# Performance work log

Measured on AMD Instinct MI355X. Metric: run time of the kernel, lower is better.

Reference implementation:

```python
import jax, jax.numpy as jnp
import numpy as np

B, S, D = 2, 2048, 1024  # batch, seq, model_dim
E, K, H = 8, 2, 4096     # experts, top_k, expert hidden
CAP_FACTOR = 1.0


def setup_inputs() -> dict:
    key = jax.random.key(0)
    ks = jax.random.split(key, 6)
    scale_in = 1.0 / np.sqrt(D)
    scale_h = 1.0 / np.sqrt(H)
    return {
        "x": jax.random.normal(ks[0], (B, S, D), jnp.float32),
        "wg": jax.random.normal(ks[1], (D, E), jnp.float32) * scale_in,
        "w1": jax.random.normal(ks[2], (E, D, H), jnp.float32) * scale_in,
        "b1": jnp.zeros((E, H), jnp.float32),
        "w2": jax.random.normal(ks[3], (E, H, D), jnp.float32) * scale_h,
        "b2": jnp.zeros((E, D), jnp.float32),
    }


def _moe_forward(x, wg, w1, b1, w2, b2):
    Bb, Ss, Dd = x.shape
    T = Bb * Ss
    cap = int(K * CAP_FACTOR * ((T + E - 1) // E))  # Tutel capacity rule
    xt = x.reshape(T, Dd)

    # ---- gating ----
    logits = xt @ wg                      # [T, E]
    scores = jax.nn.softmax(logits, axis=-1)
    gates_k, idx_k = jax.lax.top_k(scores, K)  # [T, K]
    # normalize_gate=True: renormalize top-k gates
    gates_k = gates_k / jnp.sum(gates_k, axis=-1, keepdims=True)

    # ---- GShard-style location assignment (slot-major cumsum) ----
    masks = jax.nn.one_hot(idx_k, E, dtype=jnp.int32)           # [T, K, E]
    m = jnp.transpose(masks, (1, 0, 2)).reshape(K * T, E)       # slot-major
    locs_full = jnp.cumsum(m, axis=0) - 1                       # [K*T, E]
    loc = jnp.sum(locs_full * m, axis=-1)                       # [K*T]
    loc = loc.reshape(K, T).T                                   # [T, K]
    valid = (loc < cap).astype(xt.dtype)                        # capacity drop
    loc_c = jnp.clip(loc, 0, cap - 1)

    # ---- dispatch: scatter tokens into [E, cap, D] ----
    contrib = (xt[:, None, :] * valid[:, :, None]).reshape(T * K, Dd)
    disp = jnp.zeros((E, cap, Dd), xt.dtype)
    disp = disp.at[idx_k.reshape(-1), loc_c.reshape(-1)].add(contrib)

    # ---- grouped expert FFN ----
    h = jax.nn.relu(jnp.einsum("ecd,edh->ech", disp, w1) + b1[:, None, :])
    out = jnp.einsum("ech,ehd->ecd", h, w2) + b2[:, None, :]

    # ---- combine (postscore): gather + gate-weighted sum ----
    gathered = out[idx_k, loc_c]                                # [T, K, D]
    y = jnp.einsum("tk,tkd->td", gates_k * valid, gathered)
    return y.reshape(Bb, Ss, Dd)


def reference(x, wg, w1, b1, w2, b2):
    return _moe_forward(x, wg, w1, b1, w2, b2)
```

## Files before the change

### kernel.cpp

```cpp
#include <hip/hip_runtime.h>
#include <stdint.h>

#define NTOK 4096
#define DIM  1024
#define NEXP 8
#define HID  4096
#define CAP  1024

typedef __bf16 bf16x8 __attribute__((ext_vector_type(8)));
typedef float  f32x4  __attribute__((ext_vector_type(4)));

__device__ __forceinline__ unsigned short f2bf(float f) {
  unsigned int u = __float_as_uint(f);
  return (unsigned short)((u + 0x7fffu + ((u >> 16) & 1u)) >> 16);
}

__device__ __forceinline__ void load_lds16(const void* g, void* l) {
  __builtin_amdgcn_global_load_lds(
      (__attribute__((address_space(1))) void*)g,
      (__attribute__((address_space(3))) void*)l,
      16, 0, 0);
}

__global__ void gating_kernel(const float* __restrict__ x, const float* __restrict__ wg,
                              int* __restrict__ tok_e, float* __restrict__ tok_g) {
  const int t = blockIdx.x;
  const int l = threadIdx.x;
  float acc[NEXP];
#pragma unroll
  for (int e = 0; e < NEXP; ++e) acc[e] = 0.f;

  const float4* x4  = (const float4*)(x + (size_t)t * DIM);
  const float4* wg4 = (const float4*)wg;
#pragma unroll
  for (int i = 0; i < 4; ++i) {
    int dq = i * 64 + l;
    float4 xv = x4[dq];
    float xs[4] = {xv.x, xv.y, xv.z, xv.w};
#pragma unroll
    for (int c = 0; c < 4; ++c) {
      int d = dq * 4 + c;
      float4 wa = wg4[d * 2], wb = wg4[d * 2 + 1];
      acc[0] += xs[c] * wa.x; acc[1] += xs[c] * wa.y;
      acc[2] += xs[c] * wa.z; acc[3] += xs[c] * wa.w;
      acc[4] += xs[c] * wb.x; acc[5] += xs[c] * wb.y;
      acc[6] += xs[c] * wb.z; acc[7] += xs[c] * wb.w;
    }
  }
#pragma unroll
  for (int off = 32; off; off >>= 1)
#pragma unroll
    for (int e = 0; e < NEXP; ++e) acc[e] += __shfl_xor(acc[e], off);

  if (l == 0) {
    float m = acc[0];
#pragma unroll
    for (int e = 1; e < NEXP; ++e) m = fmaxf(m, acc[e]);
    float p[NEXP];
#pragma unroll
    for (int e = 0; e < NEXP; ++e) p[e] = __expf(acc[e] - m);
    int e0 = 0; float b0 = p[0];
#pragma unroll
    for (int e = 1; e < NEXP; ++e) if (p[e] > b0) { b0 = p[e]; e0 = e; }
    int e1 = -1; float b1v = -1.f;
#pragma unroll
    for (int e = 0; e < NEXP; ++e) if (e != e0 && p[e] > b1v) { b1v = p[e]; e1 = e; }
    float inv = 1.f / (b0 + b1v);
    tok_e[2 * t] = e0; tok_e[2 * t + 1] = e1;
    tok_g[2 * t] = b0 * inv; tok_g[2 * t + 1] = b1v * inv;
  }
}

__global__ void scan_kernel(const int* __restrict__ tok_e, int* __restrict__ tok_loc,
                            int* __restrict__ slot_map) {
  const int l = threadIdx.x;
  const unsigned long long below = (1ull << l) - 1ull;
  int base[NEXP];
#pragma unroll
  for (int e = 0; e < NEXP; ++e) base[e] = 0;

  int nxt = tok_e[((0 * 64 + l) & (NTOK - 1)) * 2 + ((0 * 64 + l) >> 12)];
  for (int it = 0; it < 128; ++it) {
    int e = nxt;
    if (it + 1 < 128) {
      int g2 = (it + 1) * 64 + l;
      nxt = tok_e[(g2 & (NTOK - 1)) * 2 + (g2 >> 12)];
    }
    int loc = 0;
#pragma unroll
    for (int ex = 0; ex < NEXP; ++ex) {
      unsigned long long msk = __ballot(e == ex);
      int off = __popcll(msk & below);
      if (e == ex) loc = base[ex] + off;
      base[ex] += __popcll(msk);
    }
    int g = it * 64 + l;
    int k = g >> 12, t = g & (NTOK - 1);
    bool valid = loc < CAP;
    tok_loc[t * 2 + k] = valid ? loc : -1;
    if (valid) slot_map[e * CAP + loc] = t;
  }
#pragma unroll
  for (int ex = 0; ex < NEXP; ++ex) {
    int c = base[ex] < CAP ? base[ex] : CAP;
    for (int i = c + l; i < CAP; i += 64) slot_map[ex * CAP + i] = -1;
  }
}

__global__ void dispatch_kernel(const float* __restrict__ x, const int* __restrict__ slot_map,
                                unsigned short* __restrict__ disp) {
  const int s = blockIdx.x;
  const int tid = threadIdx.x;
  int t = slot_map[s];
  uint2 o;
  if (t >= 0) {
    float4 v = ((const float4*)(x + (size_t)t * DIM))[tid];
    o.x = (unsigned)f2bf(v.x) | ((unsigned)f2bf(v.y) << 16);
    o.y = (unsigned)f2bf(v.z) | ((unsigned)f2bf(v.w) << 16);
  } else {
    o.x = 0u; o.y = 0u;
  }
  ((uint2*)(disp + (size_t)s * DIM))[tid] = o;
}

__global__ void transpose_cvt(const float* __restrict__ in, unsigned short* __restrict__ out,
                              int R, int C) {
  __shared__ float tile[64][65];
  const int e = blockIdx.z;
  const float* inp = in + (size_t)e * R * C;
  unsigned short* outp = out + (size_t)e * R * C;
  const int c0 = blockIdx.x * 64, r0 = blockIdx.y * 64;
  const int tx = threadIdx.x, ty = threadIdx.y;
#pragma unroll
  for (int i = 0; i < 16; ++i) {
    int r = ty + i * 4;
    tile[r][tx] = inp[(size_t)(r0 + r) * C + c0 + tx];
  }
  __syncthreads();
#pragma unroll
  for (int i = 0; i < 16; ++i) {
    int cl = ty + i * 4;
    outp[(size_t)(c0 + cl) * R + r0 + tx] = f2bf(tile[tx][cl]);
  }
}

template <bool RELU, bool BF16OUT>
__global__ __launch_bounds__(256)
void gemm_kernel(const unsigned short* __restrict__ A, const unsigned short* __restrict__ B,
                 const float* __restrict__ bias, void* __restrict__ Cv, int N, int K) {
  constexpr int M = 1024;
  const int e = blockIdx.z;
  A += (size_t)e * M * K;
  B += (size_t)e * N * K;
  bias += (size_t)e * N;
  const int n0 = blockIdx.x * 128;
  const int m0 = blockIdx.y * 128;
  const int tid = threadIdx.x;
  const int wave = tid >> 6, lane = tid & 63;
  const int wm = wave >> 1, wn = wave & 1;

  __shared__ __align__(16) unsigned short As[128 * 64];
  __shared__ __align__(16) unsigned short Bs[128 * 64];

  const int srow = lane >> 3;
  const int scol = (lane & 7) * 8;
  const unsigned short* gA = A + (size_t)(m0 + wave * 8 + srow) * K + scol;
  const unsigned short* gB = B + (size_t)(n0 + wave * 8 + srow) * K + scol;
  unsigned short* lA = As + (wave * 8) * 64;
  unsigned short* lB = Bs + (wave * 8) * 64;

  f32x4 acc[4][4] = {};

  const int quad = lane >> 4;
  const int arow = (wm * 64 + (lane & 15)) * 64 + quad * 8;
  const int brow = (wn * 64 + (lane & 15)) * 64 + quad * 8;

  for (int k0 = 0; k0 < K; k0 += 64) {
    __syncthreads();
#pragma unroll
    for (int i = 0; i < 4; ++i) {
      load_lds16(gA + (size_t)i * 32 * K, lA + i * 32 * 64);
      load_lds16(gB + (size_t)i * 32 * K, lB + i * 32 * 64);
    }
    gA += 64; gB += 64;
    __syncthreads();
#pragma unroll
    for (int kk = 0; kk < 64; kk += 32) {
      bf16x8 af[4], bfr[4];
#pragma unroll
      for (int i = 0; i < 4; ++i)
        af[i] = *reinterpret_cast<const bf16x8*>(&As[arow + i * 16 * 64 + kk]);
#pragma unroll
      for (int j = 0; j < 4; ++j)
        bfr[j] = *reinterpret_cast<const bf16x8*>(&Bs[brow + j * 16 * 64 + kk]);
#pragma unroll
      for (int i = 0; i < 4; ++i)
#pragma unroll
        for (int j = 0; j < 4; ++j)
          acc[i][j] = __builtin_amdgcn_mfma_f32_16x16x32_bf16(af[i], bfr[j], acc[i][j], 0, 0, 0);
    }
  }

  const int crow = m0 + wm * 64 + quad * 4;
  const int ccol = n0 + wn * 64 + (lane & 15);
  unsigned short* Cb = (unsigned short*)Cv + (size_t)e * M * N;
  float* Cf = (float*)Cv + (size_t)e * M * N;
#pragma unroll
  for (int j = 0; j < 4; ++j) {
    float bj = bias[ccol + j * 16];
#pragma unroll
    for (int i = 0; i < 4; ++i) {
#pragma unroll
      for (int r = 0; r < 4; ++r) {
        float v = acc[i][j][r] + bj;
        if (RELU) v = fmaxf(v, 0.f);
        size_t off = (size_t)(crow + i * 16 + r) * N + (ccol + j * 16);
        if (BF16OUT) Cb[off] = f2bf(v);
        else         Cf[off] = v;
      }
    }
  }
}

__global__ void combine_kernel(const float* __restrict__ outb, const int* __restrict__ tok_e,
                               const int* __restrict__ tok_loc, const float* __restrict__ tok_g,
                               float* __restrict__ y) {
  const int t = blockIdx.x;
  const int tid = threadIdx.x;
  int e0 = tok_e[2 * t], e1 = tok_e[2 * t + 1];
  int l0 = tok_loc[2 * t], l1 = tok_loc[2 * t + 1];
  float g0 = tok_g[2 * t], g1 = tok_g[2 * t + 1];
  float ax = 0.f, ay = 0.f, az = 0.f, aw = 0.f;
  if (l0 >= 0) {
    float4 v = ((const float4*)(outb + ((size_t)e0 * CAP + l0) * DIM))[tid];
    ax += g0 * v.x; ay += g0 * v.y; az += g0 * v.z; aw += g0 * v.w;
  }
  if (l1 >= 0) {
    float4 v = ((const float4*)(outb + ((size_t)e1 * CAP + l1) * DIM))[tid];
    ax += g1 * v.x; ay += g1 * v.y; az += g1 * v.z; aw += g1 * v.w;
  }
  float4 o; o.x = ax; o.y = ay; o.z = az; o.w = aw;
  ((float4*)(y + (size_t)t * DIM))[tid] = o;
}

extern "C" void kernel_launch(void* const* d_in, const int* in_sizes, int n_in,
                              void* d_out, int out_size, void* d_ws, size_t ws_size,
                              hipStream_t stream) {
  const float* x  = (const float*)d_in[0];
  const float* wg = (const float*)d_in[1];
  const float* w1 = (const float*)d_in[2];
  const float* b1 = (const float*)d_in[3];
  const float* w2 = (const float*)d_in[4];
  const float* b2 = (const float*)d_in[5];
  float* y = (float*)d_out;

  char* ws = (char*)d_ws;
  int*   tok_e    = (int*)(ws);
  int*   tok_loc  = (int*)(ws + 32768);
  float* tok_g    = (float*)(ws + 65536);
  int*   slot_map = (int*)(ws + 98304);
  unsigned short* disp = (unsigned short*)(ws + 131072);
  unsigned short* wbuf = (unsigned short*)(ws + 131072 + (16ull << 20));
  unsigned short* h    = (unsigned short*)(ws + 131072 + (80ull << 20));
  float*          outb = (float*)(ws + 131072 + (144ull << 20));

  gating_kernel<<<NTOK, 64, 0, stream>>>(x, wg, tok_e, tok_g);
  scan_kernel<<<1, 64, 0, stream>>>(tok_e, tok_loc, slot_map);
  dispatch_kernel<<<NEXP * CAP, 256, 0, stream>>>(x, slot_map, disp);
  transpose_cvt<<<dim3(HID / 64, DIM / 64, NEXP), dim3(64, 4), 0, stream>>>(w1, wbuf, DIM, HID);
  gemm_kernel<true, true><<<dim3(HID / 128, CAP / 128, NEXP), 256, 0, stream>>>(
      disp, wbuf, b1, h, HID, DIM);
  transpose_cvt<<<dim3(DIM / 64, HID / 64, NEXP), dim3(64, 4), 0, stream>>>(w2, wbuf, HID, DIM);
  gemm_kernel<false, false><<<dim3(DIM / 128, CAP / 128, NEXP), 256, 0, stream>>>(
      h, wbuf, b2, outb, DIM, HID);
  combine_kernel<<<NTOK, 256, 0, stream>>>(outb, tok_e, tok_loc, tok_g, y);
}
```

Before: 586.9 us.

## Double-buffer GEMM LDS, swizzle tile order, vectorize transpose, bf16 expert output

The expert GEMMs now double-buffer their LDS tiles so global-to-LDS loads for the next k-step overlap MFMA work, and they drop one barrier per iteration. Block indices are remapped into patches of four N-tiles to improve L2 reuse. The weight transpose-convert uses float4 loads and packed bf16 stores. The second GEMM writes bf16 instead of fp32, which halves output traffic and the combine's reads at some precision cost.

Measured after the change: 580.3 us. About the same (-1.1%).

```diff
diff --git a/kernel.cpp b/kernel.cpp
--- a/kernel.cpp
+++ b/kernel.cpp
@@ -13,6 +13,10 @@
 __device__ __forceinline__ unsigned short f2bf(float f) {
   unsigned int u = __float_as_uint(f);
   return (unsigned short)((u + 0x7fffu + ((u >> 16) & 1u)) >> 16);
+}
+
+__device__ __forceinline__ float bf2f(unsigned int bits16) {
+  return __uint_as_float(bits16 << 16);
 }
 
 __device__ __forceinline__ void load_lds16(const void* g, void* l) {
@@ -130,44 +134,63 @@
   const float* inp = in + (size_t)e * R * C;
   unsigned short* outp = out + (size_t)e * R * C;
   const int c0 = blockIdx.x * 64, r0 = blockIdx.y * 64;
-  const int tx = threadIdx.x, ty = threadIdx.y;
-#pragma unroll
-  for (int i = 0; i < 16; ++i) {
-    int r = ty + i * 4;
-    tile[r][tx] = inp[(size_t)(r0 + r) * C + c0 + tx];
+  const int t = threadIdx.x;
+#pragma unroll
+  for (int i = 0; i < 4; ++i) {
+    int idx = i * 256 + t;
+    int r = idx >> 4;
+    int c4 = (idx & 15) * 4;
+    float4 v = *(const float4*)(inp + (size_t)(r0 + r) * C + c0 + c4);
+    tile[r][c4 + 0] = v.x; tile[r][c4 + 1] = v.y;
+    tile[r][c4 + 2] = v.z; tile[r][c4 + 3] = v.w;
   }
   __syncthreads();
 #pragma unroll
-  for (int i = 0; i < 16; ++i) {
-    int cl = ty + i * 4;
-    outp[(size_t)(c0 + cl) * R + r0 + tx] = f2bf(tile[tx][cl]);
-  }
-}
-
-template <bool RELU, bool BF16OUT>
+  for (int i = 0; i < 4; ++i) {
+    int idx = i * 256 + t;
+    int c = idx >> 4;
+    int r4 = (idx & 15) * 4;
+    float a = tile[r4 + 0][c], b = tile[r4 + 1][c];
+    float d0 = tile[r4 + 2][c], d1 = tile[r4 + 3][c];
+    uint2 o;
+    o.x = (unsigned)f2bf(a) | ((unsigned)f2bf(b) << 16);
+    o.y = (unsigned)f2bf(d0) | ((unsigned)f2bf(d1) << 16);
+    *(uint2*)(outp + (size_t)(c0 + c) * R + r0 + r4) = o;
+  }
+}
+
+template <bool RELU, int MB, int NB>
 __global__ __launch_bounds__(256)
 void gemm_kernel(const unsigned short* __restrict__ A, const unsigned short* __restrict__ B,
-                 const float* __restrict__ bias, void* __restrict__ Cv, int N, int K) {
+                 const float* __restrict__ bias, unsigned short* __restrict__ C,
+                 int N, int K) {
   constexpr int M = 1024;
-  const int e = blockIdx.z;
+  const int bid = blockIdx.x;
+  const int e = bid / (MB * NB);
+  const int r = bid - e * (MB * NB);
+  const int patch = r / (MB * 4);
+  const int q = r - patch * (MB * 4);
+  const int mtile = q >> 2;
+  const int ntile = patch * 4 + (q & 3);
+
   A += (size_t)e * M * K;
   B += (size_t)e * N * K;
   bias += (size_t)e * N;
-  const int n0 = blockIdx.x * 128;
-  const int m0 = blockIdx.y * 128;
+  C += (size_t)e * M * N;
+  const int m0 = mtile * 128;
+  const int n0 = ntile * 128;
   const int tid = threadIdx.x;
   const int wave = tid >> 6, lane = tid & 63;
   const int wm = wave >> 1, wn = wave & 1;
 
-  __shared__ __align__(16) unsigned short As[128 * 64];
-  __shared__ __align__(16) unsigned short Bs[128 * 64];
+  __shared__ __align__(16) unsigned short As[2][128 * 64];
+  __shared__ __align__(16) unsigned short Bs[2][128 * 64];
 
   const int srow = lane >> 3;
   const int scol = (lane & 7) * 8;
   const unsigned short* gA = A + (size_t)(m0 + wave * 8 + srow) * K + scol;
   const unsigned short* gB = B + (size_t)(n0 + wave * 8 + srow) * K + scol;
-  unsigned short* lA = As + (wave * 8) * 64;
-  unsigned short* lB = Bs + (wave * 8) * 64;
+  const int lbase = (wave * 8) * 64;
 
   f32x4 acc[4][4] = {};
 
@@ -175,24 +198,34 @@
   const int arow = (wm * 64 + (lane & 15)) * 64 + quad * 8;
   const int brow = (wn * 64 + (lane & 15)) * 64 + quad * 8;
 
-  for (int k0 = 0; k0 < K; k0 += 64) {
+#pragma unroll
+  for (int i = 0; i < 4; ++i) {
+    load_lds16(gA + (size_t)i * 32 * K, &As[0][lbase + i * 32 * 64]);
+    load_lds16(gB + (size_t)i * 32 * K, &Bs[0][lbase + i * 32 * 64]);
+  }
+  gA += 64; gB += 64;
+
+  const int nIter = K >> 6;
+  for (int it = 0; it < nIter; ++it) {
+    const int cur = it & 1;
     __syncthreads();
-#pragma unroll
-    for (int i = 0; i < 4; ++i) {
-      load_lds16(gA + (size_t)i * 32 * K, lA + i * 32 * 64);
-      load_lds16(gB + (size_t)i * 32 * K, lB + i * 32 * 64);
-    }
-    gA += 64; gB += 64;
-    __syncthreads();
+    if (it + 1 < nIter) {
+#pragma unroll
+      for (int i = 0; i < 4; ++i) {
+        load_lds16(gA + (size_t)i * 32 * K, &As[cur ^ 1][lbase + i * 32 * 64]);
+        load_lds16(gB + (size_t)i * 32 * K, &Bs[cur ^ 1][lbase + i * 32 * 64]);
+      }
+      gA += 64; gB += 64;
+    }
 #pragma unroll
     for (int kk = 0; kk < 64; kk += 32) {
       bf16x8 af[4], bfr[4];
 #pragma unroll
       for (int i = 0; i < 4; ++i)
-        af[i] = *reinterpret_cast<const bf16x8*>(&As[arow + i * 16 * 64 + kk]);
+        af[i] = *reinterpret_cast<const bf16x8*>(&As[cur][arow + i * 16 * 64 + kk]);
 #pragma unroll
       for (int j = 0; j < 4; ++j)
-        bfr[j] = *reinterpret_cast<const bf16x8*>(&Bs[brow + j * 16 * 64 + kk]);
+        bfr[j] = *reinterpret_cast<const bf16x8*>(&Bs[cur][brow + j * 16 * 64 + kk]);
 #pragma unroll
       for (int i = 0; i < 4; ++i)
 #pragma unroll
@@ -203,28 +236,24 @@
 
   const int crow = m0 + wm * 64 + quad * 4;
   const int ccol = n0 + wn * 64 + (lane & 15);
-  unsigned short* Cb = (unsigned short*)Cv + (size_t)e * M * N;
-  float* Cf = (float*)Cv + (size_t)e * M * N;
 #pragma unroll
   for (int j = 0; j < 4; ++j) {
     float bj = bias[ccol + j * 16];
 #pragma unroll
     for (int i = 0; i < 4; ++i) {
 #pragma unroll
-      for (int r = 0; r < 4; ++r) {
-        float v = acc[i][j][r] + bj;
+      for (int rr = 0; rr < 4; ++rr) {
+        float v = acc[i][j][rr] + bj;
         if (RELU) v = fmaxf(v, 0.f);
-        size_t off = (size_t)(crow + i * 16 + r) * N + (ccol + j * 16);
-        if (BF16OUT) Cb[off] = f2bf(v);
-        else         Cf[off] = v;
+        C[(size_t)(crow + i * 16 + rr) * N + (ccol + j * 16)] = f2bf(v);
       }
     }
   }
 }
 
-__global__ void combine_kernel(const float* __restrict__ outb, const int* __restrict__ tok_e,
-                               const int* __restrict__ tok_loc, const float* __restrict__ tok_g,
-                               float* __restrict__ y) {
+__global__ void combine_kernel(const unsigned short* __restrict__ outb,
+                               const int* __restrict__ tok_e, const int* __restrict__ tok_loc,
+                               const float* __restrict__ tok_g, float* __restrict__ y) {
   const int t = blockIdx.x;
   const int tid = threadIdx.x;
   int e0 = tok_e[2 * t], e1 = tok_e[2 * t + 1];
@@ -232,12 +261,14 @@
   float g0 = tok_g[2 * t], g1 = tok_g[2 * t + 1];
   float ax = 0.f, ay = 0.f, az = 0.f, aw = 0.f;
   if (l0 >= 0) {
-    float4 v = ((const float4*)(outb + ((size_t)e0 * CAP + l0) * DIM))[tid];
-    ax += g0 * v.x; ay += g0 * v.y; az += g0 * v.z; aw += g0 * v.w;
+    uint2 u = ((const uint2*)(outb + ((size_t)e0 * CAP + l0) * DIM))[tid];
+    ax += g0 * bf2f(u.x & 0xffffu); ay += g0 * __uint_as_float(u.x & 0xffff0000u);
+    az += g0 * bf2f(u.y & 0xffffu); aw += g0 * __uint_as_float(u.y & 0xffff0000u);
   }
   if (l1 >= 0) {
-    float4 v = ((const float4*)(outb + ((size_t)e1 * CAP + l1) * DIM))[tid];
-    ax += g1 * v.x; ay += g1 * v.y; az += g1 * v.z; aw += g1 * v.w;
+    uint2 u = ((const uint2*)(outb + ((size_t)e1 * CAP + l1) * DIM))[tid];
+    ax += g1 * bf2f(u.x & 0xffffu); ay += g1 * __uint_as_float(u.x & 0xffff0000u);
+    az += g1 * bf2f(u.y & 0xffffu); aw += g1 * __uint_as_float(u.y & 0xffff0000u);
   }
   float4 o; o.x = ax; o.y = ay; o.z = az; o.w = aw;
   ((float4*)(y + (size_t)t * DIM))[tid] = o;
@@ -262,16 +293,14 @@
   unsigned short* disp = (unsigned short*)(ws + 131072);
   unsigned short* wbuf = (unsigned short*)(ws + 131072 + (16ull << 20));
   unsigned short* h    = (unsigned short*)(ws + 131072 + (80ull << 20));
-  float*          outb = (float*)(ws + 131072 + (144ull << 20));
+  unsigned short* outb = (unsigned short*)(ws + 131072 + (144ull << 20));
 
   gating_kernel<<<NTOK, 64, 0, stream>>>(x, wg, tok_e, tok_g);
   scan_kernel<<<1, 64, 0, stream>>>(tok_e, tok_loc, slot_map);
   dispatch_kernel<<<NEXP * CAP, 256, 0, stream>>>(x, slot_map, disp);
-  transpose_cvt<<<dim3(HID / 64, DIM / 64, NEXP), dim3(64, 4), 0, stream>>>(w1, wbuf, DIM, HID);
-  gemm_kernel<true, true><<<dim3(HID / 128, CAP / 128, NEXP), 256, 0, stream>>>(
-      disp, wbuf, b1, h, HID, DIM);
-  transpose_cvt<<<dim3(DIM / 64, HID / 64, NEXP), dim3(64, 4), 0, stream>>>(w2, wbuf, HID, DIM);
-  gemm_kernel<false, false><<<dim3(DIM / 128, CAP / 128, NEXP), 256, 0, stream>>>(
-      h, wbuf, b2, outb, DIM, HID);
+  transpose_cvt<<<dim3(HID / 64, DIM / 64, NEXP), 256, 0, stream>>>(w1, wbuf, DIM, HID);
+  gemm_kernel<true, 8, 32><<<NEXP * 8 * 32, 256, 0, stream>>>(disp, wbuf, b1, h, HID, DIM);
+  transpose_cvt<<<dim3(DIM / 64, HID / 64, NEXP), 256, 0, stream>>>(w2, wbuf, HID, DIM);
+  gemm_kernel<false, 8, 8><<<NEXP * 8 * 8, 256, 0, stream>>>(h, wbuf, b2, outb, DIM, HID);
   combine_kernel<<<NTOK, 256, 0, stream>>>(outb, tok_e, tok_loc, tok_g, y);
 }
```
